# Kernel optimization log

Measured on AMD Instinct MI355X. Metric: run time of the kernel, lower is better.

Reference implementation:

```python
import jax, jax.numpy as jnp
import numpy as np

S, TS, K, TK = 4, 2, 8, 8
EPS = 1e-5


def setup_inputs() -> dict:
    key = jax.random.key(0)
    ks = jax.random.split(key, 20)
    n, C, t, h, w = 8, 512, 8, 32, 32
    f = jnp.float32
    d = {}
    d["x"] = jax.random.normal(ks[0], (n, C, t, h, w), f)
    d["conv1_w"] = jax.random.normal(ks[1], (K, C), f) * 0.05
    d["conv1_b"] = jax.random.normal(ks[2], (K,), f) * 0.05
    d["bn1_g"] = jax.random.uniform(ks[3], (K,), f, 0.5, 1.5)
    d["bn1_b"] = jax.random.normal(ks[4], (K,), f) * 0.05
    d["bn1_m"] = jax.random.normal(ks[5], (K,), f) * 0.05
    d["bn1_v"] = jax.random.uniform(ks[6], (K,), f, 0.5, 1.5)
    d["convp_w"] = jax.random.normal(ks[7], (S * S * K, K, S), f) * 0.05
    d["convp_b"] = jax.random.normal(ks[8], (S * S * K,), f) * 0.05
    d["convq_w"] = jax.random.normal(ks[9], (S * S * K, K, S), f) * 0.05
    d["convq_b"] = jax.random.normal(ks[10], (S * S * K,), f) * 0.05
    d["convt_w"] = jax.random.normal(ks[11], (TS * TS * TK, K, TS), f) * 0.05
    d["convt_b"] = jax.random.normal(ks[12], (TS * TS * TK,), f) * 0.05
    d["conv2_w"] = jax.random.normal(ks[13], (C, C), f) * 0.05
    d["conv2_b"] = jax.random.normal(ks[14], (C,), f) * 0.05
    d["bn2_g"] = jax.random.uniform(ks[15], (C,), f, 0.5, 1.5)
    d["bn2_b"] = jax.random.normal(ks[16], (C,), f) * 0.05
    d["bn2_m"] = jax.random.normal(ks[17], (C,), f) * 0.05
    d["bn2_v"] = jax.random.uniform(ks[18], (C,), f, 0.5, 1.5)
    return d


def _bn(x, g, b, m, v):
    # inference-mode BatchNorm3d over channel axis 1
    sh = (1, -1, 1, 1, 1)
    return (x - m.reshape(sh)) * (g / jnp.sqrt(v + EPS)).reshape(sh) + b.reshape(sh)


def reference(x, conv1_w, conv1_b, bn1_g, bn1_b, bn1_m, bn1_v,
              convp_w, convp_b, convq_w, convq_b, convt_w, convt_b,
              conv2_w, conv2_b, bn2_g, bn2_b, bn2_m, bn2_v):
    n, C, t, h, w = x.shape
    s, ts, k, tk = S, TS, K, TK
    hb, wb, tb = h // s, w // s, t // ts
    # conv1 (1x1x1) + BN + ReLU -> (n,k,t,h,w)
    o = jnp.einsum('oc,ncthw->nothw', conv1_w, x) + conv1_b.reshape(1, -1, 1, 1, 1)
    o = jax.nn.relu(_bn(o, bn1_g, bn1_b, bn1_m, bn1_v))
    # adaptive max pools: (t,s,1) and (t,1,s) -> (n,k,t,s)
    rp = o.reshape(n, k, t, s, hb, w).max(axis=(4, 5))
    cp = o.reshape(n, k, t, h, s, wb).max(axis=(3, 5))
    # conv_p / conv_q: kernel [1,s,1] / [1,1,s] collapse the s axis
    p = (jnp.einsum('oci,ncti->not', convp_w, rp) + convp_b[None, :, None]).reshape(n, k, s, s, t)
    q = (jnp.einsum('oci,ncti->not', convq_w, cp) + convq_b[None, :, None]).reshape(n, k, s, s, t)
    p = jax.nn.softmax(p, axis=3)
    q = jax.nn.softmax(q, axis=2)
    # expand across C//k channel groups, move t forward -> (n,C,t,s,s)
    g = C // k
    P = jnp.broadcast_to(p.transpose(0, 1, 4, 2, 3)[:, :, None], (n, k, g, t, s, s)).reshape(n, C, t, s, s)
    Q = jnp.broadcast_to(q.transpose(0, 1, 4, 2, 3)[:, :, None], (n, k, g, t, s, s)).reshape(n, C, t, s, s)
    # y = kron(P, I_hb) @ x @ kron(Q, I_wb)  (resize_mat is kron with identity;
    # exploit block structure instead of materializing (n,C,t,h,h) matrices)
    xr = x.reshape(n, C, t, s, hb, w)
    y = jnp.einsum('nctab,nctbuw->nctauw', P, xr).reshape(n, C, t, h, w)
    yr = y.reshape(n, C, t, h, s, wb)
    y = jnp.einsum('ncthav,nctab->ncthbv', yr, Q).reshape(n, C, t, h, w)
    # temporal mixing: adaptive avg pool to (ts,1,1), conv_t, softmax, kron(TM, I_tb)
    tp = o.reshape(n, k, ts, tb, h, w).mean(axis=(3, 4, 5))  # (n,k,ts)
    tm = jnp.einsum('oci,nci->no', convt_w, tp) + convt_b[None, :]
    tm = jax.nn.softmax(tm.reshape(n, tk, ts, ts), axis=3)
    TM = jnp.broadcast_to(tm[:, :, None], (n, tk, C // tk, ts, ts)).reshape(n, C, ts, ts)
    y = jnp.einsum('ncab,ncbuhw->ncauhw', TM, y.reshape(n, C, ts, tb, h, w)).reshape(n, C, t, h, w)
    # conv2 (1x1x1) + BN + ReLU
    y = jnp.einsum('oc,ncthw->nothw', conv2_w, y) + conv2_b.reshape(1, -1, 1, 1, 1)
    return jax.nn.relu(_bn(y, bn2_g, bn2_b, bn2_m, bn2_v))
```

## Files before the change

### kernel.cpp

```cpp
#include <hip/hip_runtime.h>
#include <math.h>

#define EPS 1e-5f

typedef __bf16 bf16x8 __attribute__((ext_vector_type(8)));
typedef float f32x4 __attribute__((ext_vector_type(4)));

__device__ static inline unsigned short f2bf(float f) {
    unsigned u = __float_as_uint(f);
    unsigned r = (u + 0x7fffu + ((u >> 16) & 1u)) >> 16;
    return (unsigned short)r;
}

__device__ static inline void load_lds16(const void* g, void* l) {
    __builtin_amdgcn_global_load_lds(
        (const __attribute__((address_space(1))) unsigned int*)g,
        (__attribute__((address_space(3))) unsigned int*)l, 16, 0, 0);
}

__global__ __launch_bounds__(512) void k_conv1_pool(
    const float* __restrict__ x,  const float* __restrict__ w1,
    const float* __restrict__ b1, const float* __restrict__ g1,
    const float* __restrict__ bb1,const float* __restrict__ m1,
    const float* __restrict__ v1,
    const float* __restrict__ w2, unsigned short* __restrict__ w2bf,
    float* __restrict__ rp, float* __restrict__ cp, float* __restrict__ tps)
{
    const int a   = blockIdx.x;
    const int t   = blockIdx.y;
    const int nn  = blockIdx.z;
    const int tid = threadIdx.x;
    const int wv  = tid >> 6;
    const int lane= tid & 63;

    __shared__ float part[8 * 8 * 256];

    {
        int gid = (((nn * 8 + t) * 4 + a) * 512) + tid;
        if (gid < 65536) {
            float4 v = *(const float4*)&w2[gid * 4];
            ushort4 o;
            o.x = f2bf(v.x); o.y = f2bf(v.y); o.z = f2bf(v.z); o.w = f2bf(v.w);
            *(ushort4*)&w2bf[gid * 4] = o;
        }
    }

    const int cbase = __builtin_amdgcn_readfirstlane(wv) * 64;
    const float* xb = x + (size_t)nn * 512 * 8192 + (size_t)cbase * 8192
                        + t * 1024 + a * 256 + lane * 4;
    const float* wb = w1 + cbase;

    f32x4 acc[8];
#pragma unroll
    for (int k = 0; k < 8; k++) acc[k] = (f32x4){0.f, 0.f, 0.f, 0.f};

    for (int c = 0; c < 64; c += 8) {
        float4 xv[8];
#pragma unroll
        for (int cc = 0; cc < 8; cc++)
            xv[cc] = *(const float4*)(xb + (size_t)(c + cc) * 8192);
#pragma unroll
        for (int cc = 0; cc < 8; cc++) {
#pragma unroll
            for (int k = 0; k < 8; k++) {
                float wt = wb[k * 512 + c + cc];
                acc[k][0] += wt * xv[cc].x;
                acc[k][1] += wt * xv[cc].y;
                acc[k][2] += wt * xv[cc].z;
                acc[k][3] += wt * xv[cc].w;
            }
        }
    }
#pragma unroll
    for (int k = 0; k < 8; k++)
        *(f32x4*)&part[(wv * 8 + k) * 256 + lane * 4] = acc[k];
    __syncthreads();

    {
        const int k = tid >> 6;
        f32x4 s = (f32x4){0.f, 0.f, 0.f, 0.f};
#pragma unroll
        for (int g = 0; g < 8; g++) {
            f32x4 p = *(const f32x4*)&part[(g * 8 + k) * 256 + lane * 4];
            s[0] += p[0]; s[1] += p[1]; s[2] += p[2]; s[3] += p[3];
        }
        const float sc = g1[k] * rsqrtf(v1[k] + EPS);
        const float ba = (b1[k] - m1[k]) * sc + bb1[k];
        float o0 = fmaxf(s[0] * sc + ba, 0.f);
        float o1 = fmaxf(s[1] * sc + ba, 0.f);
        float o2 = fmaxf(s[2] * sc + ba, 0.f);
        float o3 = fmaxf(s[3] * sc + ba, 0.f);

        float m4 = fmaxf(fmaxf(o0, o1), fmaxf(o2, o3));
        float s4 = o0 + o1 + o2 + o3;

        float mr = m4;
#pragma unroll
        for (int m = 32; m >= 1; m >>= 1) mr = fmaxf(mr, __shfl_xor(mr, m, 64));
        if (lane == 0) rp[((nn * 8 + k) * 8 + t) * 4 + a] = mr;

        float mc = m4;
        mc = fmaxf(mc, __shfl_xor(mc, 1, 64));
        mc = fmaxf(mc, __shfl_xor(mc, 8, 64));
        mc = fmaxf(mc, __shfl_xor(mc, 16, 64));
        mc = fmaxf(mc, __shfl_xor(mc, 32, 64));
        if ((lane & 0x39) == 0)
            atomicMax((int*)&cp[((nn * 8 + k) * 8 + t) * 4 + (lane >> 1)],
                      __float_as_int(mc));

        float ss = s4;
#pragma unroll
        for (int m = 32; m >= 1; m >>= 1) ss += __shfl_xor(ss, m, 64);
        if (lane == 0) atomicAdd(&tps[(nn * 8 + k) * 2 + (t >> 2)], ss);
    }
}

__global__ __launch_bounds__(256) void k_pqtm(
    const float* __restrict__ rp, const float* __restrict__ cp,
    const float* __restrict__ tps,
    const float* __restrict__ pw, const float* __restrict__ pb,
    const float* __restrict__ qw, const float* __restrict__ qb,
    const float* __restrict__ tw, const float* __restrict__ tbv,
    float* __restrict__ P, float* __restrict__ Q, float* __restrict__ TM)
{
    const int nn  = blockIdx.x;
    const int tid = threadIdx.x;
    __shared__ float rps[256], cps[256], tpss[16];
    rps[tid] = rp[nn * 256 + tid];
    cps[tid] = cp[nn * 256 + tid];
    if (tid < 16) tpss[tid] = tps[nn * 16 + tid] * (1.0f / 4096.0f);
    __syncthreads();

    {
        int k = tid >> 5, a = (tid >> 3) & 3, t = tid & 7;
        float v[4];
#pragma unroll
        for (int b = 0; b < 4; b++) {
            int o = k * 16 + a * 4 + b;
            float s = pb[o];
#pragma unroll
            for (int c = 0; c < 8; c++)
#pragma unroll
                for (int i = 0; i < 4; i++)
                    s += pw[o * 32 + c * 4 + i] * rps[c * 32 + t * 4 + i];
            v[b] = s;
        }
        float mx = fmaxf(fmaxf(v[0], v[1]), fmaxf(v[2], v[3]));
        float e[4]; float sum = 0.f;
#pragma unroll
        for (int b = 0; b < 4; b++) { e[b] = expf(v[b] - mx); sum += e[b]; }
        float inv = 1.f / sum;
        int base = ((nn * 8 + k) * 8 + t) * 16 + a * 4;
#pragma unroll
        for (int b = 0; b < 4; b++) P[base + b] = e[b] * inv;
    }
    {
        int k = tid >> 5, b = (tid >> 3) & 3, t = tid & 7;
        float v[4];
#pragma unroll
        for (int a = 0; a < 4; a++) {
            int o = k * 16 + a * 4 + b;
            float s = qb[o];
#pragma unroll
            for (int c = 0; c < 8; c++)
#pragma unroll
                for (int i = 0; i < 4; i++)
                    s += qw[o * 32 + c * 4 + i] * cps[c * 32 + t * 4 + i];
            v[a] = s;
        }
        float mx = fmaxf(fmaxf(v[0], v[1]), fmaxf(v[2], v[3]));
        float e[4]; float sum = 0.f;
#pragma unroll
        for (int a = 0; a < 4; a++) { e[a] = expf(v[a] - mx); sum += e[a]; }
        float inv = 1.f / sum;
        int base = ((nn * 8 + k) * 8 + t) * 16 + b;
#pragma unroll
        for (int a = 0; a < 4; a++) Q[base + a * 4] = e[a] * inv;
    }
    if (tid < 16) {
        int kk = tid >> 1, a2 = tid & 1;
        float v[2];
#pragma unroll
        for (int b2 = 0; b2 < 2; b2++) {
            int o = kk * 4 + a2 * 2 + b2;
            float s = tbv[o];
#pragma unroll
            for (int c = 0; c < 8; c++)
#pragma unroll
                for (int i = 0; i < 2; i++)
                    s += tw[o * 16 + c * 2 + i] * tpss[c * 2 + i];
            v[b2] = s;
        }
        float mx = fmaxf(v[0], v[1]);
        float e0 = expf(v[0] - mx), e1 = expf(v[1] - mx);
        float inv = 1.f / (e0 + e1);
        TM[nn * 32 + kk * 4 + a2 * 2 + 0] = e0 * inv;
        TM[nn * 32 + kk * 4 + a2 * 2 + 1] = e1 * inv;
    }
}

__global__ __launch_bounds__(256) void k_mix(
    const float* __restrict__ x, const float* __restrict__ P,
    const float* __restrict__ Q, const float* __restrict__ TM,
    unsigned short* __restrict__ y3T)
{
    const int u2  = blockIdx.x >> 3;
    const int u   = blockIdx.x & 7;
    const int cg  = blockIdx.y;
    const int nn  = blockIdx.z;
    const int tid = threadIdx.x;
    const int kc  = cg >> 1;

    __shared__ float xs[8192];
    __shared__ unsigned short ys[8192];

    const size_t xbase = (size_t)nn * 512 * 8192 + (size_t)cg * 32 * 8192;
#pragma unroll
    for (int rr = 0; rr < 8; rr++) {
        int id  = rr * 256 + tid;
        int row = id >> 3;
        int jw  = (id & 7) ^ (row & 7);
        int tt = row >> 7, b = (row >> 5) & 3, c = row & 31;
        const float* src = x + xbase + (size_t)c * 8192
                             + (u2 + 4 * tt) * 1024 + (b * 8 + u) * 32 + jw * 4;
        *(float4*)&xs[id * 4] = *(const float4*)src;
    }

    const int a = tid >> 6, vh = (tid >> 5) & 1, c = tid & 31;
    float Pt[2][4], Qt[2][4][4];
#pragma unroll
    for (int tt = 0; tt < 2; tt++) {
        const float* Pb = &P[((nn * 8 + kc) * 8 + (u2 + 4 * tt)) * 16];
        const float* Qb = &Q[((nn * 8 + kc) * 8 + (u2 + 4 * tt)) * 16];
#pragma unroll
        for (int b = 0; b < 4; b++) Pt[tt][b] = Pb[a * 4 + b];
#pragma unroll
        for (int aw = 0; aw < 4; aw++)
#pragma unroll
            for (int bw = 0; bw < 4; bw++) Qt[tt][aw][bw] = Qb[aw * 4 + bw];
    }
    const float* TMb = &TM[nn * 32 + kc * 4];
    const float tm00 = TMb[0], tm01 = TMb[1], tm10 = TMb[2], tm11 = TMb[3];
    __syncthreads();

    float y1[2][4][4];
#pragma unroll
    for (int tt = 0; tt < 2; tt++)
#pragma unroll
        for (int aw = 0; aw < 4; aw++)
#pragma unroll
            for (int vi = 0; vi < 4; vi++) y1[tt][aw][vi] = 0.f;
#pragma unroll
    for (int tt = 0; tt < 2; tt++) {
#pragma unroll
        for (int b = 0; b < 4; b++) {
            float pv = Pt[tt][b];
            int row = (tt * 4 + b) * 32 + c;
#pragma unroll
            for (int aw = 0; aw < 4; aw++) {
                int slot = (aw * 2 + vh) ^ (c & 7);
                float4 xv = *(const float4*)&xs[(row * 8 + slot) * 4];
                y1[tt][aw][0] += pv * xv.x;
                y1[tt][aw][1] += pv * xv.y;
                y1[tt][aw][2] += pv * xv.z;
                y1[tt][aw][3] += pv * xv.w;
            }
        }
    }
#pragma unroll
    for (int bw = 0; bw < 4; bw++) {
#pragma unroll
        for (int vi = 0; vi < 4; vi++) {
            float s0 = 0.f, s1 = 0.f;
#pragma unroll
            for (int aw = 0; aw < 4; aw++) {
                s0 += Qt[0][aw][bw] * y1[0][aw][vi];
                s1 += Qt[1][aw][bw] * y1[1][aw][vi];
            }
            int wout = bw * 8 + vh * 4 + vi;
            ys[((0 + a) * 32 + wout) * 32 + c] = f2bf(tm00 * s0 + tm01 * s1);
            ys[((4 + a) * 32 + wout) * 32 + c] = f2bf(tm10 * s0 + tm11 * s1);
        }
    }
    __syncthreads();

#pragma unroll
    for (int it = 0; it < 4; it++) {
        int id  = it * 256 + tid;
        int row = id >> 2, jc = id & 3;
        int tt = row >> 7, aa = (row >> 5) & 3, w = row & 31;
        int p = (u2 + 4 * tt) * 1024 + (aa * 8 + u) * 32 + w;
        uint4 val = *(const uint4*)&ys[row * 32 + jc * 8];
        *(uint4*)&y3T[((size_t)nn * 8192 + p) * 512 + cg * 32 + jc * 8] = val;
    }
}

__global__ __launch_bounds__(256) void k_gemm2(
    const unsigned short* __restrict__ y3T,
    const unsigned short* __restrict__ w2bf,
    const float* __restrict__ b2, const float* __restrict__ g2,
    const float* __restrict__ bb2,const float* __restrict__ m2,
    const float* __restrict__ v2, float* __restrict__ out)
{
    const int ct  = blockIdx.x;
    const int pt  = blockIdx.y;
    const int nn  = blockIdx.z;
    const int tid = threadIdx.x;
    const int co0 = ct * 128, p0 = pt * 128;

    __shared__ unsigned short As[8192];
    __shared__ unsigned short Bs[8192];
    __shared__ float sc_s[128], ba_s[128];

    if (tid < 128) {
        int co = co0 + tid;
        float sc = g2[co] * rsqrtf(v2[co] + EPS);
        sc_s[tid] = sc;
        ba_s[tid] = (b2[co] - m2[co]) * sc + bb2[co];
    }

    const int lane = tid & 63, wv = tid >> 6;
    const int wr = wv >> 1, wc = wv & 1;
    const int ln15 = lane & 15, quad = lane >> 4;

    const int lrow = lane >> 3;
    const int jc   = (lane & 7) ^ lrow;

    f32x4 acc[4][4];
#pragma unroll
    for (int i = 0; i < 4; i++)
#pragma unroll
        for (int j = 0; j < 4; j++) acc[i][j] = (f32x4){0.f, 0.f, 0.f, 0.f};

    const unsigned short* Ag = w2bf + (size_t)co0 * 512;
    const unsigned short* Bg = y3T + ((size_t)nn * 8192 + p0) * 512;

    for (int c0 = 0; c0 < 512; c0 += 64) {
#pragma unroll
        for (int it = 0; it < 4; it++) {
            int rb = (wv * 4 + it) * 8;
            load_lds16(Ag + (size_t)(rb + lrow) * 512 + c0 + jc * 8,
                       &As[(wv * 4 + it) * 512]);
            load_lds16(Bg + (size_t)(rb + lrow) * 512 + c0 + jc * 8,
                       &Bs[(wv * 4 + it) * 512]);
        }
        __syncthreads();

#pragma unroll
        for (int ks = 0; ks < 2; ks++) {
            bf16x8 a[4], b[4];
#pragma unroll
            for (int mi = 0; mi < 4; mi++) {
                int row = wr * 64 + mi * 16 + ln15;
                int chunk = row * 8 + ((ks * 4 + quad) ^ (row & 7));
                a[mi] = *(const bf16x8*)&As[chunk * 8];
            }
#pragma unroll
            for (int pi = 0; pi < 4; pi++) {
                int row = wc * 64 + pi * 16 + ln15;
                int chunk = row * 8 + ((ks * 4 + quad) ^ (row & 7));
                b[pi] = *(const bf16x8*)&Bs[chunk * 8];
            }
#pragma unroll
            for (int mi = 0; mi < 4; mi++)
#pragma unroll
                for (int pi = 0; pi < 4; pi++)
                    acc[mi][pi] = __builtin_amdgcn_mfma_f32_16x16x32_bf16(
                        a[mi], b[pi], acc[mi][pi], 0, 0, 0);
        }
        __syncthreads();
    }

#pragma unroll
    for (int mi = 0; mi < 4; mi++) {
        int lco = wr * 64 + mi * 16 + quad * 4;
#pragma unroll
        for (int pi = 0; pi < 4; pi++) {
            int p = p0 + wc * 64 + pi * 16 + ln15;
#pragma unroll
            for (int r = 0; r < 4; r++) {
                float vv = fmaxf(acc[mi][pi][r] * sc_s[lco + r] + ba_s[lco + r],
                                 0.f);
                __builtin_nontemporal_store(
                    vv, &out[((size_t)nn * 512 + co0 + lco + r) * 8192 + p]);
            }
        }
    }
}

extern "C" void kernel_launch(void* const* d_in, const int* in_sizes, int n_in,
                              void* d_out, int out_size, void* d_ws, size_t ws_size,
                              hipStream_t stream) {
    const float* x   = (const float*)d_in[0];
    const float* w1  = (const float*)d_in[1];
    const float* b1  = (const float*)d_in[2];
    const float* g1  = (const float*)d_in[3];
    const float* bb1 = (const float*)d_in[4];
    const float* m1  = (const float*)d_in[5];
    const float* v1  = (const float*)d_in[6];
    const float* pw  = (const float*)d_in[7];
    const float* pb  = (const float*)d_in[8];
    const float* qw  = (const float*)d_in[9];
    const float* qb  = (const float*)d_in[10];
    const float* tw  = (const float*)d_in[11];
    const float* tbv = (const float*)d_in[12];
    const float* w2  = (const float*)d_in[13];
    const float* b2  = (const float*)d_in[14];
    const float* g2  = (const float*)d_in[15];
    const float* bb2 = (const float*)d_in[16];
    const float* m2  = (const float*)d_in[17];
    const float* v2  = (const float*)d_in[18];

    float* ws  = (float*)d_ws;
    float* rp  = ws;
    float* cp  = ws + 2048;
    float* tps = ws + 4096;
    float* P   = ws + 8192;
    float* Q   = ws + 16384;
    float* TM  = ws + 24576;
    unsigned short* w2bf = (unsigned short*)(ws + 32768);
    unsigned short* y3T  = (unsigned short*)(ws + 163840);

    hipMemsetAsync(ws, 0, 4224 * sizeof(float), stream);

    k_conv1_pool<<<dim3(4, 8, 8), 512, 0, stream>>>(x, w1, b1, g1, bb1, m1, v1,
                                                    w2, w2bf, rp, cp, tps);
    k_pqtm<<<dim3(8), 256, 0, stream>>>(rp, cp, tps, pw, pb, qw, qb, tw, tbv,
                                        P, Q, TM);
    k_mix<<<dim3(32, 16, 8), 256, 0, stream>>>(x, P, Q, TM, y3T);
    k_gemm2<<<dim3(4, 64, 8), 256, 0, stream>>>(y3T, w2bf, b2, g2, bb2, m2, v2,
                                                (float*)d_out);
}
```

Before: 349.7 us.

## Double-buffer conv1 channel loads via global_load_lds and split output channels per wave

Result: no change. 348.0 us (-0.5%).

```diff
diff --git a/kernel.cpp b/kernel.cpp
--- a/kernel.cpp
+++ b/kernel.cpp
@@ -33,7 +33,7 @@
     const int wv  = tid >> 6;
     const int lane= tid & 63;
 
-    __shared__ float part[8 * 8 * 256];
+    __shared__ float xs[2][8192];
 
     {
         int gid = (((nn * 8 + t) * 4 + a) * 512) + tid;
@@ -45,51 +45,48 @@
         }
     }
 
-    const int cbase = __builtin_amdgcn_readfirstlane(wv) * 64;
-    const float* xb = x + (size_t)nn * 512 * 8192 + (size_t)cbase * 8192
-                        + t * 1024 + a * 256 + lane * 4;
-    const float* wb = w1 + cbase;
-
-    f32x4 acc[8];
-#pragma unroll
-    for (int k = 0; k < 8; k++) acc[k] = (f32x4){0.f, 0.f, 0.f, 0.f};
-
-    for (int c = 0; c < 64; c += 8) {
-        float4 xv[8];
-#pragma unroll
-        for (int cc = 0; cc < 8; cc++)
-            xv[cc] = *(const float4*)(xb + (size_t)(c + cc) * 8192);
-#pragma unroll
-        for (int cc = 0; cc < 8; cc++) {
-#pragma unroll
-            for (int k = 0; k < 8; k++) {
-                float wt = wb[k * 512 + c + cc];
-                acc[k][0] += wt * xv[cc].x;
-                acc[k][1] += wt * xv[cc].y;
-                acc[k][2] += wt * xv[cc].z;
-                acc[k][3] += wt * xv[cc].w;
-            }
-        }
-    }
-#pragma unroll
-    for (int k = 0; k < 8; k++)
-        *(f32x4*)&part[(wv * 8 + k) * 256 + lane * 4] = acc[k];
+    const int k = __builtin_amdgcn_readfirstlane(wv);
+    const float* xg = x + (size_t)nn * 512 * 8192 + t * 1024 + a * 256 + lane * 4;
+
+#pragma unroll
+    for (int i = 0; i < 4; i++) {
+        int r = i * 8 + wv;
+        load_lds16(xg + (size_t)r * 8192, &xs[0][r * 256]);
+    }
     __syncthreads();
 
+    f32x4 acc = (f32x4){0.f, 0.f, 0.f, 0.f};
+    const float* wk = w1 + k * 512;
+
+    for (int ch = 0; ch < 16; ch++) {
+        const int cur = ch & 1;
+        if (ch < 15) {
+#pragma unroll
+            for (int i = 0; i < 4; i++) {
+                int r = i * 8 + wv;
+                load_lds16(xg + (size_t)((ch + 1) * 32 + r) * 8192,
+                           &xs[cur ^ 1][r * 256]);
+            }
+        }
+#pragma unroll
+        for (int c = 0; c < 32; c++) {
+            f32x4 xv = *(const f32x4*)&xs[cur][c * 256 + lane * 4];
+            float wt = wk[ch * 32 + c];
+            acc[0] += wt * xv[0];
+            acc[1] += wt * xv[1];
+            acc[2] += wt * xv[2];
+            acc[3] += wt * xv[3];
+        }
+        __syncthreads();
+    }
+
     {
-        const int k = tid >> 6;
-        f32x4 s = (f32x4){0.f, 0.f, 0.f, 0.f};
-#pragma unroll
-        for (int g = 0; g < 8; g++) {
-            f32x4 p = *(const f32x4*)&part[(g * 8 + k) * 256 + lane * 4];
-            s[0] += p[0]; s[1] += p[1]; s[2] += p[2]; s[3] += p[3];
-        }
         const float sc = g1[k] * rsqrtf(v1[k] + EPS);
         const float ba = (b1[k] - m1[k]) * sc + bb1[k];
-        float o0 = fmaxf(s[0] * sc + ba, 0.f);
-        float o1 = fmaxf(s[1] * sc + ba, 0.f);
-        float o2 = fmaxf(s[2] * sc + ba, 0.f);
-        float o3 = fmaxf(s[3] * sc + ba, 0.f);
+        float o0 = fmaxf(acc[0] * sc + ba, 0.f);
+        float o1 = fmaxf(acc[1] * sc + ba, 0.f);
+        float o2 = fmaxf(acc[2] * sc + ba, 0.f);
+        float o3 = fmaxf(acc[3] * sc + ba, 0.f);
 
         float m4 = fmaxf(fmaxf(o0, o1), fmaxf(o2, o3));
         float s4 = o0 + o1 + o2 + o3;
@@ -221,9 +218,9 @@
         int row = id >> 3;
         int jw  = (id & 7) ^ (row & 7);
         int tt = row >> 7, b = (row >> 5) & 3, c = row & 31;
-        const float* src = x + xbase + (size_t)c * 8192
-                             + (u2 + 4 * tt) * 1024 + (b * 8 + u) * 32 + jw * 4;
-        *(float4*)&xs[id * 4] = *(const float4*)src;
+        load_lds16(x + xbase + (size_t)c * 8192
+                     + (u2 + 4 * tt) * 1024 + (b * 8 + u) * 32 + jw * 4,
+                   &xs[(rr * 256 + (tid & 192)) * 4]);
     }
 
     const int a = tid >> 6, vh = (tid >> 5) & 1, c = tid & 31;
```
